# Kernel optimization log

Hardware: AMD Instinct MI355X
Metric: run time of the kernel (lower is better)

## Reference

```python
import jax, jax.numpy as jnp
import numpy as np

V, C, DFF, NH, NL, KS, OUT = 256, 192, 768, 2, 6, 3, 192
B, T, W = 64, 512, 4
DH = C // NH
PAD = KS // 2
DN = ('NCH', 'OIH', 'NCH')


def _rel_to_abs(x):
    # [b,h,l,2l-1] -> [b,h,l,l]  (VITS _relative_position_to_absolute_position)
    b, h, l, _ = x.shape
    x = jnp.pad(x, ((0, 0), (0, 0), (0, 0), (0, 1)))
    x = x.reshape(b, h, l * 2 * l)
    x = jnp.pad(x, ((0, 0), (0, 0), (0, l - 1)))
    x = x.reshape(b, h, l + 1, 2 * l - 1)
    return x[:, :, :l, l - 1:]


def _abs_to_rel(x):
    # [b,h,l,l] -> [b,h,l,2l-1]  (VITS _absolute_position_to_relative_position)
    b, h, l, _ = x.shape
    x = jnp.pad(x, ((0, 0), (0, 0), (0, 0), (0, l - 1)))
    x = x.reshape(b, h, l * (2 * l - 1))
    x = jnp.pad(x, ((0, 0), (0, 0), (l, 0)))
    x = x.reshape(b, h, l, 2 * l)
    return x[:, :, :, 1:]


def _get_rel_emb(emb, length):
    # emb: [2W+1, DH] -> [2*length-1, DH]
    pad_len = max(length - (W + 1), 0)
    start = max(W + 1 - length, 0)
    padded = jnp.pad(emb, ((pad_len, pad_len), (0, 0)))
    return padded[start:start + 2 * length - 1]


def _ln(x, g, b):
    mu = jnp.mean(x, -1, keepdims=True)
    var = jnp.mean(jnp.square(x - mu), -1, keepdims=True)
    return (x - mu) * jax.lax.rsqrt(var + 1e-5) * g + b


def setup_inputs():
    key = jax.random.key(0)
    ks = jax.random.split(key, 12)
    n = lambda k, s, std: jax.random.normal(k, s, jnp.float32) * std
    return dict(
        tokens=jax.random.randint(ks[0], (B, T), 0, V),
        x_lengths=jnp.full((B,), T, dtype=jnp.int32),
        emb_w=n(ks[1], (V, C), C ** -0.5),
        wqkv=n(ks[2], (NL, 3, C, C), 0.02),
        bqkv=jnp.zeros((NL, 3, C), jnp.float32),
        wo=n(ks[3], (NL, C, C), 0.02),
        bo=jnp.zeros((NL, C), jnp.float32),
        rel_k=n(ks[4], (NL, 2 * W + 1, DH), DH ** -0.5),
        rel_v=n(ks[5], (NL, 2 * W + 1, DH), DH ** -0.5),
        ln1_g=jnp.ones((NL, C), jnp.float32),
        ln1_b=jnp.zeros((NL, C), jnp.float32),
        ln2_g=jnp.ones((NL, C), jnp.float32),
        ln2_b=jnp.zeros((NL, C), jnp.float32),
        ffn_w1=n(ks[6], (NL, DFF, C, KS), 0.02),
        ffn_b1=jnp.zeros((NL, DFF), jnp.float32),
        ffn_w2=n(ks[7], (NL, C, DFF, KS), 0.02),
        ffn_b2=jnp.zeros((NL, C), jnp.float32),
        proj_w=n(ks[8], (2 * OUT, C), 0.02),
        proj_b=jnp.zeros((2 * OUT,), jnp.float32),
    )


def reference(tokens, x_lengths, emb_w, wqkv, bqkv, wo, bo, rel_k, rel_v,
              ln1_g, ln1_b, ln2_g, ln2_b, ffn_w1, ffn_b1, ffn_w2, ffn_b2,
              proj_w, proj_b):
    x = emb_w[tokens] * (C ** 0.5)                       # [B,T,C]
    mask = (jnp.arange(T)[None, :] < x_lengths[:, None]).astype(x.dtype)  # [B,T]
    bias = jnp.where((mask[:, None, :, None] * mask[:, None, None, :]) > 0.0, 0.0, -1e4)
    x = x * mask[..., None]
    inv_sqrt_d = DH ** -0.5
    for l in range(NL):
        q = jnp.einsum('btc,oc->bto', x, wqkv[l, 0]) + bqkv[l, 0]
        k = jnp.einsum('btc,oc->bto', x, wqkv[l, 1]) + bqkv[l, 1]
        v = jnp.einsum('btc,oc->bto', x, wqkv[l, 2]) + bqkv[l, 2]
        q = q.reshape(B, T, NH, DH).transpose(0, 2, 1, 3)  # [B,H,T,D]
        k = k.reshape(B, T, NH, DH).transpose(0, 2, 1, 3)
        v = v.reshape(B, T, NH, DH).transpose(0, 2, 1, 3)
        scores = jnp.einsum('bhtd,bhsd->bhts', q, k) * inv_sqrt_d
        rk = _get_rel_emb(rel_k[l], T)                     # [2T-1, D]
        rel_logits = jnp.einsum('bhtd,md->bhtm', q * inv_sqrt_d, rk)
        scores = scores + _rel_to_abs(rel_logits)
        p = jax.nn.softmax(scores + bias, axis=-1)
        o = jnp.einsum('bhts,bhsd->bhtd', p, v)
        o = o + jnp.einsum('bhtm,md->bhtd', _abs_to_rel(p), _get_rel_emb(rel_v[l], T))
        o = o.transpose(0, 2, 1, 3).reshape(B, T, C)
        y = jnp.einsum('btc,oc->bto', o, wo[l]) + bo[l]
        x = _ln(x + y, ln1_g[l], ln1_b[l])
        h = jax.lax.conv_general_dilated((x * mask[..., None]).transpose(0, 2, 1),
                                         ffn_w1[l], (1,), [(PAD, PAD)],
                                         dimension_numbers=DN) + ffn_b1[l][None, :, None]
        h = jax.nn.relu(h) * mask[:, None, :]
        h = jax.lax.conv_general_dilated(h, ffn_w2[l], (1,), [(PAD, PAD)],
                                         dimension_numbers=DN) + ffn_b2[l][None, :, None]
        y = h.transpose(0, 2, 1) * mask[..., None]
        x = _ln(x + y, ln2_g[l], ln2_b[l])
    x = x * mask[..., None]
    stats = (jnp.einsum('btc,oc->bto', x, proj_w) + proj_b) * mask[..., None]
    m, logs = jnp.split(stats, 2, axis=-1)
    x_mask = mask[:, None, :]
    return x.transpose(0, 2, 1), m.transpose(0, 2, 1), logs.transpose(0, 2, 1), x_mask
```

## Files before the change

### kernel.cpp

```cpp
#include <hip/hip_runtime.h>
#include <hip/hip_bf16.h>

typedef __hip_bfloat16 bf16;
typedef __attribute__((ext_vector_type(8))) short short8;
typedef __attribute__((ext_vector_type(4))) float f32x4;

#define NB 64
#define NT 512
#define NC 192
#define NHEAD 2
#define NDH 96
#define NLAYER 6
#define NDFF 768
#define NW 4

constexpr int MROWS = NB * NT;
constexpr size_t MC = (size_t)MROWS * NC;
constexpr size_t MCB = MC * 4;
constexpr float QSC = 0.10206207261596575f * 1.4426950408889634f;

__device__ __forceinline__ float us2f(unsigned short x) { return __uint_as_float((unsigned)x << 16); }
__device__ __forceinline__ unsigned short f2b(float f) {
    bf16 h = __float2bfloat16(f);
    return *reinterpret_cast<unsigned short*>(&h);
}

__global__ __launch_bounds__(256) void cvt_frag_plain(const float* __restrict__ s, bf16* __restrict__ d,
                                                      int L, int N, int K) {
    int i = blockIdx.x * 256 + threadIdx.x;
    int total = L * (N / 16) * (K / 32) * 64;
    if (i >= total) return;
    int lane = i & 63;
    int tile = i >> 6;
    int nbk = K / 32;
    int kb = tile % nbk;
    int rest = tile / nbk;
    int nb = rest % (N / 16);
    int l = rest / (N / 16);
    int li = lane & 15, g = lane >> 4;
    const float* src = s + ((size_t)l * N + nb * 16 + li) * K + kb * 32 + g * 8;
    bf16* dst = d + (size_t)i * 8;
#pragma unroll
    for (int u = 0; u < 8; u++) dst[u] = __float2bfloat16(src[u]);
}
__global__ __launch_bounds__(256) void cvt_frag_conv(const float* __restrict__ s, bf16* __restrict__ d,
                                                     int L, int N, int C) {
    int i = blockIdx.x * 256 + threadIdx.x;
    int total = L * 3 * (N / 16) * (C / 32) * 64;
    if (i >= total) return;
    int lane = i & 63;
    int tile = i >> 6;
    int nbk = C / 32;
    int kb = tile % nbk;
    int rest = tile / nbk;
    int nb = rest % (N / 16);
    int rest2 = rest / (N / 16);
    int dk = rest2 % 3;
    int l = rest2 / 3;
    int li = lane & 15, g = lane >> 4;
    const float* src = s + (((size_t)l * N + nb * 16 + li) * C + kb * 32 + g * 8) * 3 + dk;
    bf16* dst = d + (size_t)i * 8;
#pragma unroll
    for (int u = 0; u < 8; u++) dst[u] = __float2bfloat16(src[u * 3]);
}

__global__ __launch_bounds__(256) void embed_kernel(const int* __restrict__ tok,
                                                    const int* __restrict__ lens,
                                                    const float* __restrict__ emb,
                                                    float* __restrict__ x,
                                                    bf16* __restrict__ xb) {
    int idx = blockIdx.x * 256 + threadIdx.x;
    if (idx >= (int)MC) return;
    int c = idx % NC;
    int m = idx / NC;
    int t = m % NT, b = m / NT;
    float v = emb[tok[m] * NC + c] * 13.856406460551018f;
    if (t >= lens[b]) v = 0.f;
    x[idx] = v;
    xb[idx] = __float2bfloat16(v);
}

enum GMode { GM_QKV = 0, GM_CONV1 = 2, GM_PROJ = 4 };

template <int MODE, int NTOT, int KC, int TAPS>
__global__ __launch_bounds__(256) void gemm_mfma(const bf16* __restrict__ A,
                                                 const bf16* __restrict__ W,
                                                 const float* __restrict__ bias,
                                                 const int* __restrict__ lens,
                                                 float* __restrict__ of,
                                                 bf16* __restrict__ ob1,
                                                 bf16* __restrict__ ob2,
                                                 bf16* __restrict__ ob3) {
    constexpr int RA = (TAPS == 3) ? 130 : 128;
    constexpr int NBN = NTOT / 16;
    constexpr int NBK = KC / 32;
    __shared__ unsigned short As[RA * 40];
    const int tid = threadIdx.x;
    const int w = tid >> 6, lane = tid & 63;
    const int g = lane >> 4, li = lane & 15;
    const int n0 = blockIdx.x * 64;
    const int m0 = blockIdx.y * 128;
    const int b = m0 >> 9, t0 = m0 & 511;
    const int len = lens[b];
    const int nbBase = n0 >> 4;
    const unsigned short* Au = (const unsigned short*)A;
    const unsigned short* Wu = (const unsigned short*)W;

    f32x4 acc[2][4];
#pragma unroll
    for (int a = 0; a < 2; a++)
#pragma unroll
        for (int s = 0; s < 4; s++) acc[a][s] = (f32x4){0.f, 0.f, 0.f, 0.f};

#pragma unroll 1
    for (int k0 = 0; k0 < KC; k0 += 32) {
        const int kb = k0 >> 5;
        __syncthreads();
        for (int c = tid; c < RA * 2; c += 256) {
            int i = c >> 1, hf = (c & 1) * 16;
            int t = t0 + i - (TAPS == 3 ? 1 : 0);
            bool valid = (t >= 0) && (t < NT);
            if constexpr (MODE == GM_CONV1) valid = valid && (t < len);
            short8 v0{}, v1{};
            if (valid) {
                const unsigned short* src = Au + ((size_t)(b * NT + t) * KC + k0 + hf);
                v0 = *(const short8*)src;
                v1 = *(const short8*)(src + 8);
            }
            *(short8*)&As[i * 40 + hf] = v0;
            *(short8*)&As[i * 40 + hf + 8] = v1;
        }
        __syncthreads();
#pragma unroll
        for (int dk = 0; dk < TAPS; dk++) {
            short8 af0 = *(const short8*)&As[(w * 32 + li + dk) * 40 + g * 8];
            short8 af1 = *(const short8*)&As[(w * 32 + 16 + li + dk) * 40 + g * 8];
#pragma unroll
            for (int sub = 0; sub < 4; sub++) {
                short8 bfr = *(const short8*)(Wu +
                    ((((size_t)(dk * NBN + nbBase + sub)) * NBK + kb) << 9) + (lane << 3));
                acc[0][sub] = __builtin_amdgcn_mfma_f32_16x16x32_bf16(af0, bfr, acc[0][sub], 0, 0, 0);
                acc[1][sub] = __builtin_amdgcn_mfma_f32_16x16x32_bf16(af1, bfr, acc[1][sub], 0, 0, 0);
            }
        }
    }

#pragma unroll
    for (int sub = 0; sub < 4; sub++) {
        int n = n0 + sub * 16 + li;
        float bv = bias[n];
#pragma unroll
        for (int a = 0; a < 2; a++) {
#pragma unroll
            for (int rr = 0; rr < 4; rr++) {
                int t = t0 + w * 32 + a * 16 + g * 4 + rr;
                size_t m = (size_t)(b * NT + t);
                float vv = acc[a][sub][rr] + bv;
                if constexpr (MODE == GM_QKV) {
                    int iw = n / NC;
                    int cc = n - iw * NC;
                    int hh = cc >= NDH ? 1 : 0;
                    int d = cc - hh * NDH;
                    int bh = b * NHEAD + hh;
                    if (iw == 0) ob1[((size_t)bh * NT + t) * NDH + d] = __float2bfloat16(vv * QSC);
                    else if (iw == 1) ob2[((size_t)bh * NT + t) * NDH + d] = __float2bfloat16(vv);
                    else ob3[((size_t)bh * NDH + d) * NT + t] = __float2bfloat16(vv);
                } else if constexpr (MODE == GM_CONV1) {
                    vv = vv > 0.f ? vv : 0.f;
                    if (t >= len) vv = 0.f;
                    ob1[m * NDFF + n] = __float2bfloat16(vv);
                } else {
                    if (t >= len) vv = 0.f;
                    int half = n >= 192 ? 1 : 0;
                    int cc = n - half * 192;
                    of[(size_t)(half + 1) * MC + ((size_t)b * NC + cc) * NT + t] = vv;
                }
            }
        }
    }
}

template <int KC, int TAPS, bool MASKY, int BM>
__global__ __launch_bounds__(512, 4) void gemm_ln(const bf16* __restrict__ A,
                                                  const bf16* __restrict__ W,
                                                  const float* __restrict__ bias,
                                                  const int* __restrict__ lens,
                                                  const float* __restrict__ lng,
                                                  const float* __restrict__ lnb,
                                                  float* __restrict__ x,
                                                  bf16* __restrict__ xb) {
    constexpr int RA = BM + ((TAPS == 3) ? 2 : 0);
    constexpr int NSTEP = KC / 32;
    constexpr int NBN = 12;
    constexpr int NBK = KC / 32;
    constexpr int AR = BM / 32;
    __shared__ unsigned short As[RA * 40];
    __shared__ float rsm[BM][4];
    __shared__ float rsq[BM][4];
    const int tid = threadIdx.x;
    const int lane = tid & 63;
    const int g = lane >> 4, li = lane & 15;
    const int w = tid >> 6;
    const int wr = w & 1, wc = w >> 1;
    const int m0 = blockIdx.x * BM;
    const int b = m0 >> 9, t0 = m0 & 511;
    const int len = lens[b];
    const unsigned short* Au = (const unsigned short*)A;
    const unsigned short* Wu = (const unsigned short*)W;

    const int ai = tid >> 1, ahf = (tid & 1) * 16;
    const int at = t0 + ai - (TAPS == 3 ? 1 : 0);
    const bool aon = (tid < RA * 2);
    const bool avalid = aon && (at >= 0) && (at < NT);

    short8 ra0{}, ra1{};
    short8 bcur[TAPS][3], bnxt[TAPS][3];

    f32x4 acc[AR][3];
#pragma unroll
    for (int ar = 0; ar < AR; ar++)
#pragma unroll
        for (int sub = 0; sub < 3; sub++) acc[ar][sub] = (f32x4){0.f, 0.f, 0.f, 0.f};

    if (avalid) {
        const unsigned short* src = Au + ((size_t)(b * NT + at) * KC + 0 + ahf);
        ra0 = *(const short8*)src;
        ra1 = *(const short8*)(src + 8);
    }
#pragma unroll
    for (int dk = 0; dk < TAPS; dk++)
#pragma unroll
        for (int sub = 0; sub < 3; sub++)
            bcur[dk][sub] = *(const short8*)(Wu +
                ((((size_t)(dk * NBN + wc * 3 + sub)) * NBK) << 9) + (lane << 3));
    if (aon) {
        short8 z{};
        *(short8*)&As[ai * 40 + ahf] = avalid ? ra0 : z;
        *(short8*)&As[ai * 40 + ahf + 8] = avalid ? ra1 : z;
    }

#pragma unroll 1
    for (int s = 0; s < NSTEP; s++) {
        __syncthreads();
        if (s + 1 < NSTEP) {
            int k0 = (s + 1) * 32;
            if (avalid) {
                const unsigned short* src = Au + ((size_t)(b * NT + at) * KC + k0 + ahf);
                ra0 = *(const short8*)src;
                ra1 = *(const short8*)(src + 8);
            }
#pragma unroll
            for (int dk = 0; dk < TAPS; dk++)
#pragma unroll
                for (int sub = 0; sub < 3; sub++)
                    bnxt[dk][sub] = *(const short8*)(Wu +
                        ((((size_t)(dk * NBN + wc * 3 + sub)) * NBK + (s + 1)) << 9) + (lane << 3));
        }
#pragma unroll
        for (int dk = 0; dk < TAPS; dk++) {
            short8 af[AR];
#pragma unroll
            for (int ar = 0; ar < AR; ar++)
                af[ar] = *(const short8*)&As[(wr * (BM / 2) + ar * 16 + li + dk) * 40 + g * 8];
#pragma unroll
            for (int sub = 0; sub < 3; sub++) {
#pragma unroll
                for (int ar = 0; ar < AR; ar++)
                    acc[ar][sub] = __builtin_amdgcn_mfma_f32_16x16x32_bf16(af[ar], bcur[dk][sub], acc[ar][sub], 0, 0, 0);
            }
        }
        __syncthreads();
        if (s + 1 < NSTEP) {
            if (aon) {
                short8 z{};
                *(short8*)&As[ai * 40 + ahf] = avalid ? ra0 : z;
                *(short8*)&As[ai * 40 + ahf + 8] = avalid ? ra1 : z;
            }
#pragma unroll
            for (int dk = 0; dk < TAPS; dk++)
#pragma unroll
                for (int sub = 0; sub < 3; sub++) bcur[dk][sub] = bnxt[dk][sub];
        }
    }

    float biasv[3], gv[3], bbv[3];
#pragma unroll
    for (int sub = 0; sub < 3; sub++) {
        int n = wc * 48 + sub * 16 + li;
        biasv[sub] = bias[n];
        gv[sub] = lng[n];
        bbv[sub] = lnb[n];
    }
    float psm[AR][4], psq[AR][4];
#pragma unroll
    for (int ar = 0; ar < AR; ar++) {
#pragma unroll
        for (int rr = 0; rr < 4; rr++) {
            int r = wr * (BM / 2) + ar * 16 + 4 * g + rr;
            int t = t0 + r;
            size_t m = (size_t)(b * NT + t);
            float sm = 0.f, sq = 0.f;
#pragma unroll
            for (int sub = 0; sub < 3; sub++) {
                int n = wc * 48 + sub * 16 + li;
                float y = acc[ar][sub][rr] + biasv[sub];
                if (MASKY && t >= len) y = 0.f;
                float rres = y + x[m * NC + n];
                acc[ar][sub][rr] = rres;
                sm += rres;
                sq += rres * rres;
            }
            psm[ar][rr] = sm;
            psq[ar][rr] = sq;
        }
    }
#pragma unroll
    for (int off = 1; off < 16; off <<= 1) {
#pragma unroll
        for (int ar = 0; ar < AR; ar++)
#pragma unroll
            for (int rr = 0; rr < 4; rr++) {
                psm[ar][rr] += __shfl_xor(psm[ar][rr], off);
                psq[ar][rr] += __shfl_xor(psq[ar][rr], off);
            }
    }
    if (li == 0) {
#pragma unroll
        for (int ar = 0; ar < AR; ar++)
#pragma unroll
            for (int rr = 0; rr < 4; rr++) {
                int r = wr * (BM / 2) + ar * 16 + 4 * g + rr;
                rsm[r][wc] = psm[ar][rr];
                rsq[r][wc] = psq[ar][rr];
            }
    }
    __syncthreads();
#pragma unroll
    for (int ar = 0; ar < AR; ar++) {
#pragma unroll
        for (int rr = 0; rr < 4; rr++) {
            int r = wr * (BM / 2) + ar * 16 + 4 * g + rr;
            int t = t0 + r;
            size_t m = (size_t)(b * NT + t);
            float sm = rsm[r][0] + rsm[r][1] + rsm[r][2] + rsm[r][3];
            float sq = rsq[r][0] + rsq[r][1] + rsq[r][2] + rsq[r][3];
            float mu = sm * (1.f / NC);
            float var = fmaxf(sq * (1.f / NC) - mu * mu, 0.f);
            float rs = rsqrtf(var + 1e-5f);
#pragma unroll
            for (int sub = 0; sub < 3; sub++) {
                int n = wc * 48 + sub * 16 + li;
                float o = (acc[ar][sub][rr] - mu) * rs * gv[sub] + bbv[sub];
                x[m * NC + n] = o;
                xb[m * NC + n] = __float2bfloat16(o);
            }
        }
    }
}

__global__ __launch_bounds__(256, 4) void attn_mfma(const bf16* __restrict__ q,
                                                    const bf16* __restrict__ k,
                                                    const bf16* __restrict__ v,
                                                    const float* __restrict__ relk,
                                                    const float* __restrict__ relv,
                                                    const int* __restrict__ lens,
                                                    bf16* __restrict__ o) {
    __shared__ __align__(16) char pool[40448];
    unsigned short* Kt = (unsigned short*)pool;
    unsigned short* Vt = (unsigned short*)(pool + 13312);
    unsigned short* Pt = (unsigned short*)(pool + 27136);
    unsigned short* Pb = (unsigned short*)(pool + 36352);
    unsigned short* Qt = (unsigned short*)pool;
    unsigned short* Rk = (unsigned short*)(pool + 13312);

    const int bh = blockIdx.x, qt = blockIdx.y;
    const int b = bh >> 1, h = bh & 1;
    const int q0 = qt * 64;
    const int tid = threadIdx.x;
    const int w = tid >> 6, lane = tid & 63;
    const int g = lane >> 4, li = lane & 15;
    const int len = lens[b];
    const bool anymask = (len < NT);

    const unsigned short* qg = (const unsigned short*)q + (size_t)bh * NT * NDH;
    const unsigned short* kg = (const unsigned short*)k + (size_t)bh * NT * NDH;
    const unsigned short* vg = (const unsigned short*)v + (size_t)bh * NDH * NT;

    for (int c = tid; c < 64 * 12; c += 256) {
        int r = c / 12, seg = (c % 12) * 8;
        *(short8*)&Qt[r * 104 + seg] = *(const short8*)(qg + (size_t)(q0 + r) * NDH + seg);
    }
    for (int c = tid; c < 16 * 96; c += 256) {
        int dd = c / 96, d = c - (c / 96) * 96;
        Rk[dd * 104 + d] = (dd < 9) ? f2b(relk[dd * 96 + d]) : (unsigned short)0;
    }
    for (int c = tid; c < 4 * 16 * 32; c += 256) Pb[c] = 0;
    __syncthreads();

    f32x4 racc = (f32x4){0.f, 0.f, 0.f, 0.f};
    short8 qf[3];
#pragma unroll
    for (int kk = 0; kk < 3; kk++) {
        qf[kk] = *(const short8*)&Qt[(w * 16 + li) * 104 + kk * 32 + g * 8];
        short8 bfr = *(const short8*)&Rk[li * 104 + kk * 32 + g * 8];
        racc = __builtin_amdgcn_mfma_f32_16x16x32_bf16(qf[kk], bfr, racc, 0, 0, 0);
    }
    short8 rvf[6];
#pragma unroll
    for (int ds = 0; ds < 6; ds++) {
#pragma unroll
        for (int i = 0; i < 8; i++) {
            int j = g * 8 + i;
            int d = ds * 16 + li;
            unsigned short u = (j < 9) ? f2b(relv[j * 96 + d]) : (unsigned short)0;
            rvf[ds][i] = (short)u;
        }
    }
    __syncthreads();

    float m_run[4], l_run[4];
    f32x4 Oa[6];
#pragma unroll
    for (int rr = 0; rr < 4; rr++) { m_run[rr] = -1e30f; l_run[rr] = 0.f; }
#pragma unroll
    for (int ds = 0; ds < 6; ds++) Oa[ds] = (f32x4){0.f, 0.f, 0.f, 0.f};

    const int wrow0 = q0 + w * 16;

    for (int s0 = 0; s0 < NT; s0 += 64) {
        for (int c = tid; c < 64 * 12; c += 256) {
            int ss = c / 12, seg = (c % 12) * 8;
            *(short8*)&Kt[ss * 104 + seg] = *(const short8*)(kg + (size_t)(s0 + ss) * NDH + seg);
        }
        for (int c = tid; c < 96 * 8; c += 256) {
            int d = c >> 3, seg = (c & 7) * 8;
            *(short8*)&Vt[d * 72 + seg] = *(const short8*)(vg + (size_t)d * NT + s0 + seg);
        }
        __syncthreads();

        const bool band = (s0 <= wrow0 + 15 + NW) && (s0 + 63 >= wrow0 - NW);

        f32x4 acc[4];
#pragma unroll
        for (int sub = 0; sub < 4; sub++) acc[sub] = (f32x4){0.f, 0.f, 0.f, 0.f};
        __builtin_amdgcn_s_setprio(1);
#pragma unroll
        for (int kk = 0; kk < 3; kk++) {
#pragma unroll
            for (int sub = 0; sub < 4; sub++) {
                short8 bfr = *(const short8*)&Kt[(sub * 16 + li) * 104 + kk * 32 + g * 8];
                acc[sub] = __builtin_amdgcn_mfma_f32_16x16x32_bf16(qf[kk], bfr, acc[sub], 0, 0, 0);
            }
        }
        __builtin_amdgcn_s_setprio(0);

        if (band) {
#pragma unroll
            for (int sub = 0; sub < 4; sub++) {
#pragma unroll
                for (int rr = 0; rr < 4; rr++) {
                    int scol = s0 + sub * 16 + li;
                    int qrow = wrow0 + 4 * g + rr;
                    int dd = scol - qrow;
                    float rv = __shfl(racc[rr], g * 16 + dd + NW);
                    if (dd >= -NW && dd <= NW) acc[sub][rr] += rv;
                }
            }
        }
        float rmax[4];
#pragma unroll
        for (int rr = 0; rr < 4; rr++) rmax[rr] = -1e30f;
#pragma unroll
        for (int sub = 0; sub < 4; sub++) {
#pragma unroll
            for (int rr = 0; rr < 4; rr++) {
                if (anymask) {
                    int scol = s0 + sub * 16 + li;
                    int qrow = wrow0 + 4 * g + rr;
                    if (scol >= len || qrow >= len) acc[sub][rr] -= 14427.0f;
                }
                rmax[rr] = fmaxf(rmax[rr], acc[sub][rr]);
            }
        }
#pragma unroll
        for (int off = 1; off < 16; off <<= 1)
#pragma unroll
            for (int rr = 0; rr < 4; rr++) rmax[rr] = fmaxf(rmax[rr], __shfl_xor(rmax[rr], off));

        float growth = -3.0e38f;
#pragma unroll
        for (int rr = 0; rr < 4; rr++) growth = fmaxf(growth, rmax[rr] - m_run[rr]);
        if (__any(growth > 11.54f)) {
#pragma unroll
            for (int rr = 0; rr < 4; rr++) {
                float mn = fmaxf(m_run[rr], rmax[rr]);
                float scf = exp2f(m_run[rr] - mn);
                m_run[rr] = mn;
                l_run[rr] *= scf;
#pragma unroll
                for (int ds = 0; ds < 6; ds++) Oa[ds][rr] *= scf;
            }
        }
        float rsum[4] = {0.f, 0.f, 0.f, 0.f};
#pragma unroll
        for (int sub = 0; sub < 4; sub++)
#pragma unroll
            for (int rr = 0; rr < 4; rr++) {
                float p = exp2f(acc[sub][rr] - m_run[rr]);
                acc[sub][rr] = p;
                rsum[rr] += p;
            }
#pragma unroll
        for (int off = 1; off < 16; off <<= 1)
#pragma unroll
            for (int rr = 0; rr < 4; rr++) rsum[rr] += __shfl_xor(rsum[rr], off);
#pragma unroll
        for (int rr = 0; rr < 4; rr++) l_run[rr] += rsum[rr];

#pragma unroll
        for (int sub = 0; sub < 4; sub++)
#pragma unroll
            for (int rr = 0; rr < 4; rr++)
                Pt[w * 1152 + (4 * g + rr) * 72 + sub * 16 + li] = f2b(acc[sub][rr]);

        __builtin_amdgcn_s_setprio(1);
#pragma unroll
        for (int kk = 0; kk < 2; kk++) {
            short8 pa = *(const short8*)&Pt[w * 1152 + li * 72 + kk * 32 + g * 8];
#pragma unroll
            for (int ds = 0; ds < 6; ds++) {
                short8 bv = *(const short8*)&Vt[(ds * 16 + li) * 72 + kk * 32 + g * 8];
                Oa[ds] = __builtin_amdgcn_mfma_f32_16x16x32_bf16(pa, bv, Oa[ds], 0, 0, 0);
            }
        }
        __builtin_amdgcn_s_setprio(0);

        if (band) {
            for (int j = g; j < 9; j += 4) {
                int u = wrow0 + li + j - NW - s0;
                unsigned short pv_ = (u >= 0 && u < 64) ? Pt[w * 1152 + li * 72 + u] : (unsigned short)0;
                Pb[w * 512 + li * 32 + j] = pv_;
            }
            short8 pband = *(const short8*)&Pb[w * 512 + li * 32 + g * 8];
#pragma unroll
            for (int ds = 0; ds < 6; ds++)
                Oa[ds] = __builtin_amdgcn_mfma_f32_16x16x32_bf16(pband, rvf[ds], Oa[ds], 0, 0, 0);
        }
        __syncthreads();
    }

    float invl[4];
#pragma unroll
    for (int rr = 0; rr < 4; rr++) invl[rr] = 1.f / l_run[rr];
#pragma unroll
    for (int ds = 0; ds < 6; ds++)
#pragma unroll
        for (int rr = 0; rr < 4; rr++) {
            int qrow = wrow0 + 4 * g + rr;
            o[((size_t)(b * NT + qrow)) * NC + h * 96 + ds * 16 + li] =
                __float2bfloat16(Oa[ds][rr] * invl[rr]);
        }
}

__global__ __launch_bounds__(256) void xpose_kernel(const float* __restrict__ x,
                                                    const int* __restrict__ lens,
                                                    float* __restrict__ out) {
    int idx = blockIdx.x * 256 + threadIdx.x;
    if (idx >= (int)MC) return;
    int t = idx % NT;
    int bc = idx / NT;
    int c = bc % NC;
    int b = bc / NC;
    float v = (t < lens[b]) ? x[((size_t)b * NT + t) * NC + c] : 0.f;
    out[idx] = v;
}

__global__ __launch_bounds__(256) void mask_kernel(const int* __restrict__ lens, float* __restrict__ out) {
    int idx = blockIdx.x * 256 + threadIdx.x;
    if (idx >= NB * NT) return;
    int t = idx % NT;
    int b = idx / NT;
    out[idx] = (t < lens[b]) ? 1.f : 0.f;
}

extern "C" void kernel_launch(void* const* d_in, const int* in_sizes, int n_in,
                              void* d_out, int out_size, void* d_ws, size_t ws_size,
                              hipStream_t stream) {
    (void)in_sizes; (void)n_in; (void)out_size; (void)ws_size;
    const int* tok = (const int*)d_in[0];
    const int* lens = (const int*)d_in[1];
    const float* emb = (const float*)d_in[2];
    const float* wqkv = (const float*)d_in[3];
    const float* bqkv = (const float*)d_in[4];
    const float* wo = (const float*)d_in[5];
    const float* bo = (const float*)d_in[6];
    const float* relk = (const float*)d_in[7];
    const float* relv = (const float*)d_in[8];
    const float* ln1g = (const float*)d_in[9];
    const float* ln1b = (const float*)d_in[10];
    const float* ln2g = (const float*)d_in[11];
    const float* ln2b = (const float*)d_in[12];
    const float* fw1 = (const float*)d_in[13];
    const float* fb1 = (const float*)d_in[14];
    const float* fw2 = (const float*)d_in[15];
    const float* fb2 = (const float*)d_in[16];
    const float* pw = (const float*)d_in[17];
    const float* pb = (const float*)d_in[18];
    float* out = (float*)d_out;

    char* wsb = (char*)d_ws;
    float* xB = (float*)wsb;
    bf16* xb = (bf16*)(wsb + 2 * MCB);
    bf16* qb = (bf16*)(wsb + 2 * MCB + MCB / 2);
    bf16* kb = qb + MC;
    bf16* vb = kb + MC;
    bf16* ob = vb + MC;
    bf16* hB = qb;
    bf16* pwqkv = ob + MC;
    bf16* pwo = pwqkv + (size_t)NLAYER * 3 * NC * NC;
    bf16* pw1 = pwo + (size_t)NLAYER * NC * NC;
    bf16* pw2 = pw1 + (size_t)NLAYER * 3 * NDFF * NC;
    bf16* pproj = pw2 + (size_t)NLAYER * 3 * NC * NDFF;

    {
        int n1 = NLAYER * 36 * 6 * 64;
        cvt_frag_plain<<<(n1 + 255) / 256, 256, 0, stream>>>(wqkv, pwqkv, NLAYER, 576, 192);
        int n2 = NLAYER * 12 * 6 * 64;
        cvt_frag_plain<<<(n2 + 255) / 256, 256, 0, stream>>>(wo, pwo, NLAYER, 192, 192);
        int n3 = 1 * 24 * 6 * 64;
        cvt_frag_plain<<<(n3 + 255) / 256, 256, 0, stream>>>(pw, pproj, 1, 384, 192);
        int n4 = NLAYER * 3 * 48 * 6 * 64;
        cvt_frag_conv<<<(n4 + 255) / 256, 256, 0, stream>>>(fw1, pw1, NLAYER, 768, 192);
        int n5 = NLAYER * 3 * 12 * 24 * 64;
        cvt_frag_conv<<<(n5 + 255) / 256, 256, 0, stream>>>(fw2, pw2, NLAYER, 192, 768);
    }

    embed_kernel<<<(int)((MC + 255) / 256), 256, 0, stream>>>(tok, lens, emb, xB, xb);

    for (int l = 0; l < NLAYER; l++) {
        gemm_mfma<GM_QKV, 576, 192, 1><<<dim3(9, 256), 256, 0, stream>>>(
            xb, pwqkv + (size_t)l * 3 * NC * NC, bqkv + (size_t)l * 3 * NC, lens,
            nullptr, qb, kb, vb);
        attn_mfma<<<dim3(NB * NHEAD, 8), 256, 0, stream>>>(
            qb, kb, vb, relk + (size_t)l * (2 * NW + 1) * NDH,
            relv + (size_t)l * (2 * NW + 1) * NDH, lens, ob);
        gemm_ln<192, 1, false, 64><<<512, 512, 0, stream>>>(
            ob, pwo + (size_t)l * NC * NC, bo + (size_t)l * NC, lens,
            ln1g + (size_t)l * NC, ln1b + (size_t)l * NC, xB, xb);
        gemm_mfma<GM_CONV1, 768, 192, 3><<<dim3(12, 256), 256, 0, stream>>>(
            xb, pw1 + (size_t)l * 3 * NDFF * NC, fb1 + (size_t)l * NDFF, lens,
            nullptr, hB, nullptr, nullptr);
        gemm_ln<768, 3, true, 64><<<512, 512, 0, stream>>>(
            hB, pw2 + (size_t)l * 3 * NC * NDFF, fb2 + (size_t)l * NC, lens,
            ln2g + (size_t)l * NC, ln2b + (size_t)l * NC, xB, xb);
    }

    gemm_mfma<GM_PROJ, 384, 192, 1><<<dim3(6, 256), 256, 0, stream>>>(
        xb, pproj, pb, lens, out, nullptr, nullptr, nullptr);
    xpose_kernel<<<(int)((MC + 255) / 256), 256, 0, stream>>>(xB, lens, out);
    mask_kernel<<<(NB * NT + 255) / 256, 256, 0, stream>>>(lens, out + 3 * MC);
}
```

Baseline: 1.448 ms.

## Drop fp32 residual stream for bf16 and compute softmax row-sum via MFMA

The fp32 residual copy of the hidden state is removed. The LayerNorm GEMMs now read the residual from, and write it back to, the bf16 buffer only, which halves residual memory traffic in every layer. Separately, the attention kernel drops the per-tile row-sum shuffle reduction: it accumulates the softmax denominator with an extra MFMA against a ones column and only reduces the row max when the rescale threshold trips. This risks accuracy loss from keeping the residual in bf16 across six layers, and the row max is now a lane-partial value in the common path.

```diff
diff --git a/kernel.cpp b/kernel.cpp
--- a/kernel.cpp
+++ b/kernel.cpp
@@ -67,7 +67,6 @@
 __global__ __launch_bounds__(256) void embed_kernel(const int* __restrict__ tok,
                                                     const int* __restrict__ lens,
                                                     const float* __restrict__ emb,
-                                                    float* __restrict__ x,
                                                     bf16* __restrict__ xb) {
     int idx = blockIdx.x * 256 + threadIdx.x;
     if (idx >= (int)MC) return;
@@ -76,7 +75,6 @@
     int t = m % NT, b = m / NT;
     float v = emb[tok[m] * NC + c] * 13.856406460551018f;
     if (t >= lens[b]) v = 0.f;
-    x[idx] = v;
     xb[idx] = __float2bfloat16(v);
 }
 
@@ -187,7 +185,6 @@
                                                   const int* __restrict__ lens,
                                                   const float* __restrict__ lng,
                                                   const float* __restrict__ lnb,
-                                                  float* __restrict__ x,
                                                   bf16* __restrict__ xb) {
     constexpr int RA = BM + ((TAPS == 3) ? 2 : 0);
     constexpr int NSTEP = KC / 32;
@@ -207,6 +204,7 @@
     const int len = lens[b];
     const unsigned short* Au = (const unsigned short*)A;
     const unsigned short* Wu = (const unsigned short*)W;
+    unsigned short* Xu = (unsigned short*)xb;
 
     const int ai = tid >> 1, ahf = (tid & 1) * 16;
     const int at = t0 + ai - (TAPS == 3 ? 1 : 0);
@@ -305,7 +303,7 @@
                 int n = wc * 48 + sub * 16 + li;
                 float y = acc[ar][sub][rr] + biasv[sub];
                 if (MASKY && t >= len) y = 0.f;
-                float rres = y + x[m * NC + n];
+                float rres = y + us2f(Xu[m * NC + n]);
                 acc[ar][sub][rr] = rres;
                 sm += rres;
                 sq += rres * rres;
@@ -351,8 +349,7 @@
             for (int sub = 0; sub < 3; sub++) {
                 int n = wc * 48 + sub * 16 + li;
                 float o = (acc[ar][sub][rr] - mu) * rs * gv[sub] + bbv[sub];
-                x[m * NC + n] = o;
-                xb[m * NC + n] = __float2bfloat16(o);
+                Xu[m * NC + n] = f2b(o);
             }
         }
     }
@@ -416,14 +413,17 @@
             rvf[ds][i] = (short)u;
         }
     }
+    short8 bones;
+#pragma unroll
+    for (int i = 0; i < 8; i++) bones[i] = (li == 0) ? (short)0x3F80 : (short)0;
     __syncthreads();
 
-    float m_run[4], l_run[4];
-    f32x4 Oa[6];
-#pragma unroll
-    for (int rr = 0; rr < 4; rr++) { m_run[rr] = -1e30f; l_run[rr] = 0.f; }
-#pragma unroll
-    for (int ds = 0; ds < 6; ds++) Oa[ds] = (f32x4){0.f, 0.f, 0.f, 0.f};
+    float m_run[4];
+    f32x4 Oa[7];
+#pragma unroll
+    for (int rr = 0; rr < 4; rr++) m_run[rr] = -1e30f;
+#pragma unroll
+    for (int ds = 0; ds < 7; ds++) Oa[ds] = (f32x4){0.f, 0.f, 0.f, 0.f};
 
     const int wrow0 = q0 + w * 16;
 
@@ -467,55 +467,43 @@
                 }
             }
         }
-        float rmax[4];
-#pragma unroll
-        for (int rr = 0; rr < 4; rr++) rmax[rr] = -1e30f;
-#pragma unroll
-        for (int sub = 0; sub < 4; sub++) {
-#pragma unroll
-            for (int rr = 0; rr < 4; rr++) {
-                if (anymask) {
+        if (anymask) {
+#pragma unroll
+            for (int sub = 0; sub < 4; sub++) {
+#pragma unroll
+                for (int rr = 0; rr < 4; rr++) {
                     int scol = s0 + sub * 16 + li;
                     int qrow = wrow0 + 4 * g + rr;
                     if (scol >= len || qrow >= len) acc[sub][rr] -= 14427.0f;
                 }
-                rmax[rr] = fmaxf(rmax[rr], acc[sub][rr]);
-            }
-        }
-#pragma unroll
-        for (int off = 1; off < 16; off <<= 1)
-#pragma unroll
-            for (int rr = 0; rr < 4; rr++) rmax[rr] = fmaxf(rmax[rr], __shfl_xor(rmax[rr], off));
-
-        float growth = -3.0e38f;
-#pragma unroll
-        for (int rr = 0; rr < 4; rr++) growth = fmaxf(growth, rmax[rr] - m_run[rr]);
+            }
+        }
+        float pmr[4];
+#pragma unroll
+        for (int rr = 0; rr < 4; rr++) {
+            pmr[rr] = fmaxf(fmaxf(acc[0][rr], acc[1][rr]), fmaxf(acc[2][rr], acc[3][rr]));
+        }
+        float growth = fmaxf(fmaxf(pmr[0] - m_run[0], pmr[1] - m_run[1]),
+                             fmaxf(pmr[2] - m_run[2], pmr[3] - m_run[3]));
         if (__any(growth > 11.54f)) {
 #pragma unroll
+            for (int off = 1; off < 16; off <<= 1)
+#pragma unroll
+                for (int rr = 0; rr < 4; rr++) pmr[rr] = fmaxf(pmr[rr], __shfl_xor(pmr[rr], off));
+#pragma unroll
             for (int rr = 0; rr < 4; rr++) {
-                float mn = fmaxf(m_run[rr], rmax[rr]);
+                float mn = fmaxf(m_run[rr], pmr[rr]);
                 float scf = exp2f(m_run[rr] - mn);
                 m_run[rr] = mn;
-                l_run[rr] *= scf;
-#pragma unroll
-                for (int ds = 0; ds < 6; ds++) Oa[ds][rr] *= scf;
-            }
-        }
-        float rsum[4] = {0.f, 0.f, 0.f, 0.f};
+#pragma unroll
+                for (int ds = 0; ds < 7; ds++) Oa[ds][rr] *= scf;
+            }
+        }
 #pragma unroll
         for (int sub = 0; sub < 4; sub++)
 #pragma unroll
-            for (int rr = 0; rr < 4; rr++) {
-                float p = exp2f(acc[sub][rr] - m_run[rr]);
-                acc[sub][rr] = p;
-                rsum[rr] += p;
-            }
-#pragma unroll
-        for (int off = 1; off < 16; off <<= 1)
-#pragma unroll
-            for (int rr = 0; rr < 4; rr++) rsum[rr] += __shfl_xor(rsum[rr], off);
-#pragma unroll
-        for (int rr = 0; rr < 4; rr++) l_run[rr] += rsum[rr];
+            for (int rr = 0; rr < 4; rr++)
+                acc[sub][rr] = exp2f(acc[sub][rr] - m_run[rr]);
 
 #pragma unroll
         for (int sub = 0; sub < 4; sub++)
@@ -532,6 +520,7 @@
                 short8 bv = *(const short8*)&Vt[(ds * 16 + li) * 72 + kk * 32 + g * 8];
                 Oa[ds] = __builtin_amdgcn_mfma_f32_16x16x32_bf16(pa, bv, Oa[ds], 0, 0, 0);
             }
+            Oa[6] = __builtin_amdgcn_mfma_f32_16x16x32_bf16(pa, bones, Oa[6], 0, 0, 0);
         }
         __builtin_amdgcn_s_setprio(0);
 
@@ -551,7 +540,7 @@
 
     float invl[4];
 #pragma unroll
-    for (int rr = 0; rr < 4; rr++) invl[rr] = 1.f / l_run[rr];
+    for (int rr = 0; rr < 4; rr++) invl[rr] = 1.f / __shfl(Oa[6][rr], lane & 48);
 #pragma unroll
     for (int ds = 0; ds < 6; ds++)
 #pragma unroll
@@ -562,7 +551,7 @@
         }
 }
 
-__global__ __launch_bounds__(256) void xpose_kernel(const float* __restrict__ x,
+__global__ __launch_bounds__(256) void xpose_kernel(const bf16* __restrict__ xb,
                                                     const int* __restrict__ lens,
                                                     float* __restrict__ out) {
     int idx = blockIdx.x * 256 + threadIdx.x;
@@ -571,7 +560,7 @@
     int bc = idx / NT;
     int c = bc % NC;
     int b = bc / NC;
-    float v = (t < lens[b]) ? x[((size_t)b * NT + t) * NC + c] : 0.f;
+    float v = (t < lens[b]) ? us2f(((const unsigned short*)xb)[((size_t)b * NT + t) * NC + c]) : 0.f;
     out[idx] = v;
 }
 
@@ -609,7 +598,6 @@
     float* out = (float*)d_out;
 
     char* wsb = (char*)d_ws;
-    float* xB = (float*)wsb;
     bf16* xb = (bf16*)(wsb + 2 * MCB);
     bf16* qb = (bf16*)(wsb + 2 * MCB + MCB / 2);
     bf16* kb = qb + MC;
@@ -635,7 +623,7 @@
         cvt_frag_conv<<<(n5 + 255) / 256, 256, 0, stream>>>(fw2, pw2, NLAYER, 192, 768);
     }
 
-    embed_kernel<<<(int)((MC + 255) / 256), 256, 0, stream>>>(tok, lens, emb, xB, xb);
+    embed_kernel<<<(int)((MC + 255) / 256), 256, 0, stream>>>(tok, lens, emb, xb);
 
     for (int l = 0; l < NLAYER; l++) {
         gemm_mfma<GM_QKV, 576, 192, 1><<<dim3(9, 256), 256, 0, stream>>>(
@@ -646,17 +634,17 @@
             relv + (size_t)l * (2 * NW + 1) * NDH, lens, ob);
         gemm_ln<192, 1, false, 64><<<512, 512, 0, stream>>>(
             ob, pwo + (size_t)l * NC * NC, bo + (size_t)l * NC, lens,
-            ln1g + (size_t)l * NC, ln1b + (size_t)l * NC, xB, xb);
+            ln1g + (size_t)l * NC, ln1b + (size_t)l * NC, xb);
         gemm_mfma<GM_CONV1, 768, 192, 3><<<dim3(12, 256), 256, 0, stream>>>(
             xb, pw1 + (size_t)l * 3 * NDFF * NC, fb1 + (size_t)l * NDFF, lens,
             nullptr, hB, nullptr, nullptr);
         gemm_ln<768, 3, true, 64><<<512, 512, 0, stream>>>(
             hB, pw2 + (size_t)l * 3 * NC * NDFF, fb2 + (size_t)l * NC, lens,
-            ln2g + (size_t)l * NC, ln2b + (size_t)l * NC, xB, xb);
+            ln2g + (size_t)l * NC, ln2b + (size_t)l * NC, xb);
     }
 
     gemm_mfma<GM_PROJ, 384, 192, 1><<<dim3(6, 256), 256, 0, stream>>>(
         xb, pproj, pb, lens, out, nullptr, nullptr, nullptr);
-    xpose_kernel<<<(int)((MC + 255) / 256), 256, 0, stream>>>(xB, lens, out);
+    xpose_kernel<<<(int)((MC + 255) / 256), 256, 0, stream>>>(xb, lens, out);
     mask_kernel<<<(NB * NT + 255) / 256, 256, 0, stream>>>(lens, out + 3 * MC);
 }
```

After: 1.369 ms. -5.5%, faster.
